# Optimization experiments

Measured on AMD Instinct MI355X. Metric: run time of the kernel, lower is better.

## Reference

```python
import jax, jax.numpy as jnp
import numpy as np
from jax import lax

C, K, EMB = 10, 32, 32
B, H, W = 32, 128, 128
DIRS = ((-1, 0), (1, 0), (0, -1), (0, 1))  # up, down, left, right


def _shift(x, dh, dw):
    # shift (B,H,W,...) by (dh,dw) with zero fill; x[b,h,w] <- x[b,h+dh,w+dw]
    pad = [(0, 0), (max(dh, 0), max(-dh, 0)), (max(dw, 0), max(-dw, 0))] + [(0, 0)] * (x.ndim - 3)
    xp = jnp.pad(x, pad)
    h0, w0 = max(-dh, 0), max(-dw, 0)
    return lax.dynamic_slice_in_dim(lax.dynamic_slice_in_dim(xp, h0, x.shape[1], 1), w0, x.shape[2], 2)


def conv(x, w, b):
    y = lax.conv_general_dilated(x, w, (1, 1), 'SAME',
                                 dimension_numbers=('NHWC', 'HWIO', 'NHWC'))
    return y + b


def small_cnn(x, w1, b1, w2, b2, w3, b3):
    x = jax.nn.relu(conv(x, w1, b1))
    x = jax.nn.relu(conv(x, w2, b2))
    return conv(x, w3, b3)


def neighbor_affinity(phi, tau=0.5):
    # phi: (B,H,W,D) -> w: (B,H,W,4) Gaussian feature affinity to 4 neighbors
    ones = jnp.ones(phi.shape[:3] + (1,), phi.dtype)
    ws = []
    for dh, dw in DIRS:
        nb = _shift(phi, dh, dw)
        valid = _shift(ones, dh, dw)[..., 0]
        d2 = jnp.sum((phi - nb) ** 2, axis=-1)
        ws.append(jnp.exp(-d2 / tau) * valid)
    return jnp.stack(ws, axis=-1)


def init_seeds_soft(Bv, Hv, Wv, Kv, dtype=jnp.float32):
    # K seeds on a gh x gw grid; soft assignment by squared distance
    gh = 4
    gw = Kv // gh
    sh = (jnp.arange(gh, dtype=dtype) + 0.5) * (Hv / gh)
    sw = (jnp.arange(gw, dtype=dtype) + 0.5) * (Wv / gw)
    seed_h = jnp.repeat(sh, gw)  # (K,)
    seed_w = jnp.tile(sw, gh)    # (K,)
    hh = jnp.arange(Hv, dtype=dtype)[:, None, None]
    ww = jnp.arange(Wv, dtype=dtype)[None, :, None]
    d2 = (hh - seed_h) ** 2 + (ww - seed_w) ** 2  # (H,W,K)
    sigma2 = (Hv / gh) * (Wv / gw)
    A = jax.nn.softmax(-d2 / sigma2, axis=-1)
    return jnp.broadcast_to(A[None], (Bv, Hv, Wv, Kv))


def soft_message_pass(A, w, beta=2.0):
    # aggregate neighbor assignments weighted by affinity, renormalize over K
    agg = jnp.zeros_like(A)
    for d, (dh, dw) in enumerate(DIRS):
        agg = agg + w[..., d:d + 1] * _shift(A, dh, dw)
    return jax.nn.softmax(beta * agg, axis=-1)


def soft_pool_features(G, A):
    # G:(B,H,W,C), A:(B,H,W,K) -> T:(B,K,1+2+C+4)
    Bv, Hv, Wv, Cv = G.shape
    eps = 1e-6
    mass = jnp.sum(A, axis=(1, 2)) + eps                      # (B,K)
    hh = (jnp.arange(Hv, dtype=G.dtype) + 0.5) / Hv
    ww = (jnp.arange(Wv, dtype=G.dtype) + 0.5) / Wv
    h_c = jnp.einsum('bhwk,h->bk', A, hh) / mass
    w_c = jnp.einsum('bhwk,w->bk', A, ww) / mass
    col = jnp.einsum('bhwk,bhwc->bkc', A, G) / mass[..., None]
    h2 = jnp.einsum('bhwk,h->bk', A, hh ** 2) / mass
    w2 = jnp.einsum('bhwk,w->bk', A, ww ** 2) / mass
    h_sd = jnp.sqrt(jax.nn.relu(h2 - h_c ** 2) + eps)
    w_sd = jnp.sqrt(jax.nn.relu(w2 - w_c ** 2) + eps)
    size = (mass / (Hv * Wv))[..., None]                      # (B,K,1)
    cen = jnp.stack([h_c, w_c], axis=-1)                      # (B,K,2)
    bbox = jnp.stack([h_c - h_sd, h_c + h_sd, w_c - w_sd, w_c + w_sd], axis=-1)
    return jnp.concatenate([size, cen, col, bbox], axis=-1)


def setup_inputs() -> dict:
    key = jax.random.key(0)
    ks = jax.random.split(key, 4)
    X = jax.random.randint(ks[0], (B, H, W), 0, C)
    w1 = jax.random.normal(ks[1], (3, 3, C, 32), jnp.float32) * (1.0 / np.sqrt(9 * C))
    w2 = jax.random.normal(ks[2], (3, 3, 32, 32), jnp.float32) * (1.0 / np.sqrt(9 * 32))
    w3 = jax.random.normal(ks[3], (1, 1, 32, EMB), jnp.float32) * (1.0 / np.sqrt(32))
    return {'X': X, 'w1': w1, 'b1': jnp.zeros((32,), jnp.float32),
            'w2': w2, 'b2': jnp.zeros((32,), jnp.float32),
            'w3': w3, 'b3': jnp.zeros((EMB,), jnp.float32)}


def reference(X, w1, b1, w2, b2, w3, b3):
    G = jax.nn.one_hot(X, C, dtype=jnp.float32)              # (B,H,W,C)
    phi = small_cnn(G, w1, b1, w2, b2, w3, b3)               # (B,H,W,EMB)
    w = neighbor_affinity(phi)                               # (B,H,W,4)
    A = init_seeds_soft(G.shape[0], G.shape[1], G.shape[2], K, G.dtype)
    for _ in range(8):
        A = soft_message_pass(A, w, beta=2.0)
    T = soft_pool_features(G, A)
    return A, T
```

## Files before the change

### kernel.cpp

```cpp
#include <hip/hip_runtime.h>
#include <math.h>

#define HD 128
#define WD 128
#define BB 32
#define KK 32
#define NPIX (BB*HD*WD)
#define PLANE ((size_t)NPIX*8)

typedef _Float16 f16;
typedef __attribute__((ext_vector_type(8))) _Float16 f16x8;
typedef __attribute__((ext_vector_type(4))) _Float16 f16x4;
typedef __attribute__((ext_vector_type(4))) float f32x4;

__device__ __forceinline__ int swz(int row, int g){
  return row*64 + (((g + (row >> 1)) & 3) << 4);
}

__device__ __forceinline__ float xexp2(float x){
#if __has_builtin(__builtin_amdgcn_exp2f)
  return __builtin_amdgcn_exp2f(x);
#else
  return exp2f(x);
#endif
}
__device__ __forceinline__ float xrcp(float x){
#if __has_builtin(__builtin_amdgcn_rcpf)
  return __builtin_amdgcn_rcpf(x);
#else
  return 1.f/x;
#endif
}
__device__ __forceinline__ f16x8 bc8(f16 x){
  f16x8 v;
  #pragma unroll
  for (int j = 0; j < 8; j++) v[j] = x;
  return v;
}

#define WSCALE 2.8853900817779268f

__global__ __launch_bounds__(512, 4) void cnnaff_kernel(
    const int* __restrict__ X,
    const float* __restrict__ w1, const float* __restrict__ b1,
    const float* __restrict__ w2, const float* __restrict__ b2,
    const float* __restrict__ w3, const float* __restrict__ b3,
    float* __restrict__ wb)
{
  __shared__ f16 sW1f[9*11*40];
  __shared__ int   sX[22*38];
  __shared__ float sB2[32], sB3[32];
  __shared__ f16 x1[720*32];
  __shared__ f16 w2t[9*32*32];
  __shared__ f16 w3t[32*32];

  const int tid = threadIdx.x;
  const int img = blockIdx.z;
  const int bh0 = blockIdx.y * 16;
  const int bw0 = blockIdx.x * 32;

  for (int i = tid; i < 9*11*32; i += 512) {
    int tap = i / 352, c = (i % 352) >> 5, oc = i & 31;
    float v = (c < 10) ? w1[tap*320 + c*32 + oc] : 0.f;
    if (tap == 4 && c < 10) v += b1[oc];
    sW1f[(tap*11 + c)*40 + oc] = (f16)v;
  }
  for (int i = tid; i < 9*32*32; i += 512) {
    int tap = i >> 10, ic = (i >> 5) & 31, oc = i & 31;
    int off = swz(tap*32 + oc, ic >> 3) + (ic & 7)*2;
    *(f16*)((char*)w2t + off) = (f16)w2[i];
  }
  for (int i = tid; i < 32*32; i += 512) {
    int ic = i >> 5, oe = i & 31;
    int off = swz(oe, ic >> 3) + (ic & 7)*2;
    *(f16*)((char*)w3t + off) = (f16)w3[i];
  }
  if (tid < 32) { sB2[tid] = b2[tid]; sB3[tid] = b3[tid]; }
  for (int i = tid; i < 22*38; i += 512) {
    int ti = i / 38, tj = i % 38;
    int gh = bh0 - 3 + ti, gw = bw0 - 3 + tj;
    sX[i] = (gh >= 0 && gh < HD && gw >= 0 && gw < WD) ? X[(img*HD + gh)*WD + gw] : 10;
  }
  __syncthreads();

  for (int p = tid; p < 720; p += 512) {
    int r = p / 36, c = p - r*36;
    int gh = bh0 - 2 + r, gw = bw0 - 2 + c;
    if (gh >= 0 && gh < HD && gw >= 0 && gw < WD) {
      f16x8 acc[4];
      {
        int cc = sX[r*38 + c];
        const f16* wr = &sW1f[cc*40];
        #pragma unroll
        for (int g = 0; g < 4; g++) acc[g] = *(const f16x8*)(wr + g*8);
      }
      #pragma unroll
      for (int tap = 1; tap < 9; tap++) {
        const int ti = tap/3, tj = tap%3;
        int cc = sX[(r+ti)*38 + c + tj];
        const f16* wr = &sW1f[(tap*11 + cc)*40];
        #pragma unroll
        for (int g = 0; g < 4; g++) acc[g] += *(const f16x8*)(wr + g*8);
      }
      #pragma unroll
      for (int g = 0; g < 4; g++) {
        f16x8 rr = acc[g];
        #pragma unroll
        for (int j = 0; j < 8; j++) rr[j] = (rr[j] > (f16)0.f) ? rr[j] : (f16)0.f;
        *(f16x8*)((char*)x1 + swz(p, g)) = rr;
      }
    } else {
      f16x8 z;
      #pragma unroll
      for (int j = 0; j < 8; j++) z[j] = (f16)0.f;
      #pragma unroll
      for (int g = 0; g < 4; g++) *(f16x8*)((char*)x1 + swz(p, g)) = z;
    }
  }
  __syncthreads();

  const int lane = tid & 63;
  const int wv   = tid >> 6;
  const int lr   = lane & 15;
  const int kg   = lane >> 4;
  const int mts  = wv * 5;

  int arow0[5];
  #pragma unroll
  for (int q = 0; q < 5; q++) {
    int px = (mts + q)*16 + lr;
    int pr = px / 34, pc = px - pr*34;
    arow0[q] = pr*36 + pc;
  }
  float b2v0 = sB2[lr], b2v1 = sB2[lr + 16];
  f32x4 acc[5][2];
  #pragma unroll
  for (int q = 0; q < 5; q++) {
    acc[q][0] = (f32x4){b2v0, b2v0, b2v0, b2v0};
    acc[q][1] = (f32x4){b2v1, b2v1, b2v1, b2v1};
  }
  #pragma unroll
  for (int tap = 0; tap < 9; tap++) {
    const int ti = tap/3, tj = tap%3;
    f16x8 bf0 = *(const f16x8*)((const char*)w2t + swz(tap*32 + lr,      kg));
    f16x8 bf1 = *(const f16x8*)((const char*)w2t + swz(tap*32 + lr + 16, kg));
    #pragma unroll
    for (int q = 0; q < 5; q++) {
      int row = arow0[q] + ti*36 + tj;
      f16x8 af = *(const f16x8*)((const char*)x1 + swz(row, kg));
      acc[q][0] = __builtin_amdgcn_mfma_f32_16x16x32_f16(af, bf0, acc[q][0], 0, 0, 0);
      acc[q][1] = __builtin_amdgcn_mfma_f32_16x16x32_f16(af, bf1, acc[q][1], 0, 0, 0);
    }
  }
  __syncthreads();

  #pragma unroll
  for (int q = 0; q < 5; q++)
    #pragma unroll
    for (int nt = 0; nt < 2; nt++) {
      int oc = nt*16 + lr;
      #pragma unroll
      for (int rg = 0; rg < 4; rg++) {
        int px = (mts + q)*16 + kg*4 + rg;
        int off = swz(px, oc >> 3) + (oc & 7)*2;
        *(f16*)((char*)x1 + off) = (f16)fmaxf(acc[q][nt][rg], 0.f);
      }
    }
  __syncthreads();

  {
    f16x8 cf0 = *(const f16x8*)((const char*)w3t + swz(lr,      kg));
    f16x8 cf1 = *(const f16x8*)((const char*)w3t + swz(lr + 16, kg));
    float b3v0 = sB3[lr], b3v1 = sB3[lr + 16];
    #pragma unroll
    for (int q = 0; q < 5; q++) {
      f16x8 af = *(const f16x8*)((const char*)x1 + swz((mts + q)*16 + lr, kg));
      f32x4 o0 = (f32x4){b3v0, b3v0, b3v0, b3v0};
      f32x4 o1 = (f32x4){b3v1, b3v1, b3v1, b3v1};
      o0 = __builtin_amdgcn_mfma_f32_16x16x32_f16(af, cf0, o0, 0, 0, 0);
      o1 = __builtin_amdgcn_mfma_f32_16x16x32_f16(af, cf1, o1, 0, 0, 0);
      #pragma unroll
      for (int rg = 0; rg < 4; rg++) {
        int px = (mts + q)*16 + kg*4 + rg;
        int offA = swz(px, lr >> 3) + (lr & 7)*2;
        int offB = swz(px, (lr+16) >> 3) + (lr & 7)*2;
        *(f16*)((char*)x1 + offA) = (f16)o0[rg];
        *(f16*)((char*)x1 + offB) = (f16)o1[rg];
      }
    }
  }
  __syncthreads();

  {
    int r2 = tid >> 5, c2 = tid & 31;
    int gh = bh0 + r2, gw = bw0 + c2;
    int qc = (r2+1)*34 + (c2+1);
    f16x8 c0 = *(const f16x8*)((const char*)x1 + swz(qc, 0));
    f16x8 c1 = *(const f16x8*)((const char*)x1 + swz(qc, 1));
    f16x8 c2v = *(const f16x8*)((const char*)x1 + swz(qc, 2));
    f16x8 c3 = *(const f16x8*)((const char*)x1 + swz(qc, 3));
    float4 out;
    #pragma unroll
    for (int d = 0; d < 4; d++) {
      int slot = (d == 0) ? qc + 34 : (d == 1) ? qc - 34 : (d == 2) ? qc + 1 : qc - 1;
      bool valid = (d == 0) ? (gh < HD-1) : (d == 1) ? (gh > 0) : (d == 2) ? (gw < WD-1) : (gw > 0);
      f16x8 n0 = *(const f16x8*)((const char*)x1 + swz(slot, 0));
      f16x8 n1 = *(const f16x8*)((const char*)x1 + swz(slot, 1));
      f16x8 n2 = *(const f16x8*)((const char*)x1 + swz(slot, 2));
      f16x8 n3 = *(const f16x8*)((const char*)x1 + swz(slot, 3));
      f16x8 d0 = c0 - n0; f16x8 s = d0*d0;
      f16x8 d1 = c1 - n1; s += d1*d1;
      f16x8 d2 = c2v - n2; s += d2*d2;
      f16x8 d3 = c3 - n3; s += d3*d3;
      float d2f = 0.f;
      #pragma unroll
      for (int j = 0; j < 8; j++) d2f += (float)s[j];
      float v = valid ? WSCALE * xexp2(-WSCALE * d2f) : 0.f;
      if (d == 0) out.x = v; else if (d == 1) out.y = v; else if (d == 2) out.z = v; else out.w = v;
    }
    ((float4*)wb)[(size_t)img*HD*WD + gh*WD + gw] = out;
  }
}

__device__ __forceinline__ void a0_accum2(float* a, int hh, int ww, float wt) {
  const float C = 0.0028177637517362567f;
  float eh[4], ew[8];
  float sh = 0.f, sw = 0.f;
  const float fh = (float)hh, fw = (float)ww;
  #pragma unroll
  for (int kh = 0; kh < 4; kh++) { float d = fh - (float)(kh*32+16); eh[kh] = xexp2(-d*d*C); sh += eh[kh]; }
  #pragma unroll
  for (int kw = 0; kw < 8; kw++) { float d = fw - (float)(kw*16+8); ew[kw] = xexp2(-d*d*C); sw += ew[kw]; }
  float sc = wt * xrcp(sh * sw);
  #pragma unroll
  for (int kh = 0; kh < 4; kh++) {
    float ehs = eh[kh] * sc;
    #pragma unroll
    for (int kw = 0; kw < 8; kw++) a[kh*8+kw] = fmaf(ehs, ew[kw], a[kh*8+kw]);
  }
}

template<int FIRST, int LAST>
__global__ __launch_bounds__(512, 6) void mp2_kernel(const f16* __restrict__ Ain,
                                                     const float* __restrict__ wb,
                                                     f16* __restrict__ Aout,
                                                     float* __restrict__ AoutF) {
  __shared__ f16 amid[612*32];

  const int blk  = blockIdx.x;
  const int xcd  = blk & 7;
  const int q    = blk >> 3;
  const int img  = xcd + ((q >> 5) << 3);
  const int tile = q & 31;
  const int th0  = (tile >> 2) * 16;
  const int tw0  = (tile & 3) * 32;
  const size_t ibase = (size_t)img * HD * WD;

  for (int p = threadIdx.x; p < 612; p += 512) {
    int r = p / 34, cc = p - r*34;
    int gh = th0 - 1 + r, gw = tw0 - 1 + cc;
    bool inimg = ((unsigned)gh < (unsigned)HD) && ((unsigned)gw < (unsigned)WD);
    int ghc = min(max(gh, 0), HD-1), gwc = min(max(gw, 0), WD-1);
    float4 wd = inimg ? ((const float4*)wb)[ibase + gh*WD + gw] : make_float4(0.f,0.f,0.f,0.f);
    int hu = ghc + ((ghc < HD-1) ? 1 : 0);
    int hd = ghc - ((ghc > 0)    ? 1 : 0);
    int wl = gwc + ((gwc < WD-1) ? 1 : 0);
    int wr = gwc - ((gwc > 0)    ? 1 : 0);

    float s = 0.f;
    f16x8 pe[4];
    if (FIRST) {
      float a[32];
      #pragma unroll
      for (int k = 0; k < 32; k++) a[k] = 0.f;
      a0_accum2(a, hu, gwc, wd.x);
      a0_accum2(a, hd, gwc, wd.y);
      a0_accum2(a, ghc, wl, wd.z);
      a0_accum2(a, ghc, wr, wd.w);
      #pragma unroll
      for (int g = 0; g < 4; g++)
        #pragma unroll
        for (int j = 0; j < 8; j++) { float e = xexp2(a[g*8+j]); s += e; pe[g][j] = (f16)e; }
    } else {
      const size_t iu_ = ibase + (size_t)hu*WD + gwc;
      const size_t id_ = ibase + (size_t)hd*WD + gwc;
      const size_t il_ = ibase + (size_t)ghc*WD + wl;
      const size_t ir_ = ibase + (size_t)ghc*WD + wr;
      f16x8 w0 = bc8((f16)wd.x), w1 = bc8((f16)wd.y), w2 = bc8((f16)wd.z), w3 = bc8((f16)wd.w);
      #pragma unroll
      for (int g = 0; g < 4; g++) {
        const f16* pg = Ain + (size_t)g*PLANE;
        f16x8 v0 = *(const f16x8*)(pg + iu_*8);
        f16x8 v1 = *(const f16x8*)(pg + id_*8);
        f16x8 v2 = *(const f16x8*)(pg + il_*8);
        f16x8 v3 = *(const f16x8*)(pg + ir_*8);
        f16x8 agg = v0*w0 + v1*w1 + v2*w2 + v3*w3;
        #pragma unroll
        for (int j = 0; j < 8; j++) { float e = xexp2((float)agg[j]); s += e; pe[g][j] = (f16)e; }
      }
    }
    f16x8 iv = bc8((f16)xrcp(s));
    #pragma unroll
    for (int g = 0; g < 4; g++)
      *(f16x8*)((char*)amid + swz(p, g)) = pe[g]*iv;
  }
  __syncthreads();

  {
    int r2 = threadIdx.x >> 5, c2 = threadIdx.x & 31;
    int gh = th0 + r2, gw = tw0 + c2;
    int rm = r2 + 1, cm = c2 + 1;
    float4 wd = ((const float4*)wb)[ibase + gh*WD + gw];
    int q0 = (rm + ((gh < HD-1) ? 1 : 0))*34 + cm;
    int q1 = (rm - ((gh > 0)    ? 1 : 0))*34 + cm;
    int q2 = rm*34 + cm + ((gw < WD-1) ? 1 : 0);
    int q3 = rm*34 + cm - ((gw > 0)    ? 1 : 0);
    f16x8 w0 = bc8((f16)wd.x), w1 = bc8((f16)wd.y), w2 = bc8((f16)wd.z), w3 = bc8((f16)wd.w);
    float s = 0.f;
    f16x8 pe[4];
    #pragma unroll
    for (int g = 0; g < 4; g++) {
      f16x8 v0 = *(const f16x8*)((const char*)amid + swz(q0, g));
      f16x8 v1 = *(const f16x8*)((const char*)amid + swz(q1, g));
      f16x8 v2 = *(const f16x8*)((const char*)amid + swz(q2, g));
      f16x8 v3 = *(const f16x8*)((const char*)amid + swz(q3, g));
      f16x8 agg = v0*w0 + v1*w1 + v2*w2 + v3*w3;
      #pragma unroll
      for (int j = 0; j < 8; j++) { float e = xexp2((float)agg[j]); s += e; pe[g][j] = (f16)e; }
    }
    f16x8 iv = bc8((f16)xrcp(s));
    #pragma unroll
    for (int g = 0; g < 4; g++) pe[g] = pe[g]*iv;

    if (!LAST) {
      size_t opix = ibase + (size_t)gh*WD + gw;
      #pragma unroll
      for (int g = 0; g < 4; g++)
        *(f16x8*)(Aout + (size_t)g*PLANE + opix*8) = pe[g];
    } else {
      __syncthreads();
      f16* planes = amid;
      #pragma unroll
      for (int g = 0; g < 4; g++)
        *(f16x8*)((char*)planes + (g*513 + threadIdx.x)*16) = pe[g];
      __syncthreads();
      float* obase = AoutF + ((size_t)(img*HD + th0)*WD + tw0)*32;
      #pragma unroll
      for (int rep = 0; rep < 8; rep++) {
        int flat = rep*512 + threadIdx.x;
        int row = flat >> 8;
        int within = flat & 255;
        int pxr = within >> 3;
        int kq = within & 7;
        int g = kq >> 1, half = kq & 1;
        int pxl = row*32 + pxr;
        f16x4 v = *(const f16x4*)((const char*)planes + (g*513 + pxl)*16 + half*8);
        float4 o;
        o.x = (float)v[0]; o.y = (float)v[1]; o.z = (float)v[2]; o.w = (float)v[3];
        *(float4*)(obase + (size_t)row*WD*32 + pxr*32 + kq*4) = o;
      }
    }
  }
}

__global__ __launch_bounds__(256) void pool1_kernel(const float* __restrict__ A,
                                                    const int* __restrict__ X,
                                                    float* __restrict__ part) {
  const int b = blockIdx.x, cy = blockIdx.y;
  const int k = threadIdx.x & 31, sub = threadIdx.x >> 5;
  const int h = cy*4 + (sub >> 1);
  const int w0 = (sub & 1) * 64;
  const float hh = ((float)h + 0.5f) * (1.f/128.f);
  float s0 = 0.f, sw = 0.f, sw2 = 0.f;
  float col[10];
  #pragma unroll
  for (int c = 0; c < 10; c++) col[c] = 0.f;
  const float* Arow = A + ((size_t)((b*HD + h)*WD + w0))*32 + k;
  const int*   Xrow = X + (b*HD + h)*WD + w0;
  for (int w = 0; w < 64; w++) {
    float a  = Arow[(size_t)w*32];
    float ww = ((float)(w + w0) + 0.5f) * (1.f/128.f);
    s0 += a; sw = fmaf(ww, a, sw); sw2 = fmaf(ww*ww, a, sw2);
    int x = Xrow[w];
    #pragma unroll
    for (int c = 0; c < 10; c++) col[c] += (x == c) ? a : 0.f;
  }
  __shared__ float red[8][32][15];
  float vals[15];
  vals[0] = s0; vals[1] = hh*s0; vals[2] = sw; vals[3] = hh*hh*s0; vals[4] = sw2;
  #pragma unroll
  for (int c = 0; c < 10; c++) vals[5+c] = col[c];
  #pragma unroll
  for (int q = 0; q < 15; q++) red[sub][k][q] = vals[q];
  __syncthreads();
  if (sub == 0) {
    #pragma unroll
    for (int q = 0; q < 15; q++) {
      float v = 0.f;
      #pragma unroll
      for (int s2 = 0; s2 < 8; s2++) v += red[s2][k][q];
      part[(((size_t)b*32 + cy)*32 + k)*15 + q] = v;
    }
  }
}

__global__ __launch_bounds__(256) void pool2_kernel(const float* __restrict__ part,
                                                    float* __restrict__ T) {
  const int t = blockIdx.x * 256 + threadIdx.x;
  if (t >= BB*KK) return;
  const int b = t >> 5, k = t & 31;
  float s[15];
  #pragma unroll
  for (int q = 0; q < 15; q++) s[q] = 0.f;
  for (int cy = 0; cy < 32; cy++) {
    const float* p = part + (((size_t)b*32 + cy)*32 + k)*15;
    #pragma unroll
    for (int q = 0; q < 15; q++) s[q] += p[q];
  }
  float mass = s[0] + 1e-6f;
  float inv  = 1.f / mass;
  float h_c = s[1]*inv, w_c = s[2]*inv, h2 = s[3]*inv, w2 = s[4]*inv;
  float h_sd = sqrtf(fmaxf(h2 - h_c*h_c, 0.f) + 1e-6f);
  float w_sd = sqrtf(fmaxf(w2 - w_c*w_c, 0.f) + 1e-6f);
  float* o = T + (size_t)t*17;
  o[0] = mass * (1.f/16384.f);
  o[1] = h_c; o[2] = w_c;
  #pragma unroll
  for (int c = 0; c < 10; c++) o[3+c] = s[5+c]*inv;
  o[13] = h_c - h_sd; o[14] = h_c + h_sd; o[15] = w_c - w_sd; o[16] = w_c + w_sd;
}

extern "C" void kernel_launch(void* const* d_in, const int* in_sizes, int n_in,
                              void* d_out, int out_size, void* d_ws, size_t ws_size,
                              hipStream_t stream) {
  const int*   X  = (const int*)d_in[0];
  const float* w1 = (const float*)d_in[1];
  const float* b1 = (const float*)d_in[2];
  const float* w2 = (const float*)d_in[3];
  const float* b2 = (const float*)d_in[4];
  const float* w3 = (const float*)d_in[5];
  const float* b3 = (const float*)d_in[6];

  float* out   = (float*)d_out;
  float* A_out = out;
  float* T_out = out + (size_t)NPIX * KK;

  char*  ws   = (char*)d_ws;
  f16*   bufA = (f16*)ws;
  f16*   bufB = (f16*)(ws + (size_t)32*1024*1024);
  float* wb   = (float*)(ws + (size_t)64*1024*1024);
  float* part = (float*)ws;

  cnnaff_kernel<<<dim3(WD/32, HD/16, BB), 512, 0, stream>>>(X, w1, b1, w2, b2, w3, b3, wb);

  mp2_kernel<1,0><<<1024, 512, 0, stream>>>(nullptr, wb, bufA, nullptr);
  mp2_kernel<0,0><<<1024, 512, 0, stream>>>(bufA, wb, bufB, nullptr);
  mp2_kernel<0,0><<<1024, 512, 0, stream>>>(bufB, wb, bufA, nullptr);
  mp2_kernel<0,1><<<1024, 512, 0, stream>>>(bufA, wb, nullptr, A_out);

  pool1_kernel<<<dim3(BB, 32), 256, 0, stream>>>(A_out, X, part);
  pool2_kernel<<<(BB*KK + 255)/256, 256, 0, stream>>>(part, T_out);
}
```

Before: 236.2 us.

## Fuse four message-pass iterations per kernel using halo-recompute in shared memory

```diff
diff --git a/kernel.cpp b/kernel.cpp
--- a/kernel.cpp
+++ b/kernel.cpp
@@ -222,30 +222,79 @@
   }
 }
 
-__device__ __forceinline__ void a0_accum2(float* a, int hh, int ww, float wt) {
+__device__ __forceinline__ void a0_row(float fh, float* eh, float& s){
   const float C = 0.0028177637517362567f;
-  float eh[4], ew[8];
-  float sh = 0.f, sw = 0.f;
-  const float fh = (float)hh, fw = (float)ww;
-  #pragma unroll
-  for (int kh = 0; kh < 4; kh++) { float d = fh - (float)(kh*32+16); eh[kh] = xexp2(-d*d*C); sh += eh[kh]; }
-  #pragma unroll
-  for (int kw = 0; kw < 8; kw++) { float d = fw - (float)(kw*16+8); ew[kw] = xexp2(-d*d*C); sw += ew[kw]; }
-  float sc = wt * xrcp(sh * sw);
-  #pragma unroll
-  for (int kh = 0; kh < 4; kh++) {
-    float ehs = eh[kh] * sc;
-    #pragma unroll
-    for (int kw = 0; kw < 8; kw++) a[kh*8+kw] = fmaf(ehs, ew[kw], a[kh*8+kw]);
-  }
+  s = 0.f;
+  #pragma unroll
+  for (int kh = 0; kh < 4; kh++){ float d = fh - (float)(kh*32+16); eh[kh] = xexp2(-d*d*C); s += eh[kh]; }
+}
+__device__ __forceinline__ void a0_col(float fw, float* ew, float& s){
+  const float C = 0.0028177637517362567f;
+  s = 0.f;
+  #pragma unroll
+  for (int kw = 0; kw < 8; kw++){ float d = fw - (float)(kw*16+8); ew[kw] = xexp2(-d*d*C); s += ew[kw]; }
+}
+
+__device__ __forceinline__ void mp_px_reg(const f16* __restrict__ amid, int slot,
+                                          int du, int dd, int dl, int dr,
+                                          float4 wd, f16x8* out) {
+  f16x8 w0 = bc8((f16)wd.x), w1 = bc8((f16)wd.y), w2 = bc8((f16)wd.z), w3 = bc8((f16)wd.w);
+  float s = 0.f;
+  f16x8 pe[4];
+  #pragma unroll
+  for (int g = 0; g < 4; g++) {
+    f16x8 v0 = *(const f16x8*)((const char*)amid + swz(slot + du, g));
+    f16x8 v1 = *(const f16x8*)((const char*)amid + swz(slot + dd, g));
+    f16x8 v2 = *(const f16x8*)((const char*)amid + swz(slot + dl, g));
+    f16x8 v3 = *(const f16x8*)((const char*)amid + swz(slot + dr, g));
+    f16x8 agg = v0*w0 + v1*w1 + v2*w2 + v3*w3;
+    #pragma unroll
+    for (int j = 0; j < 8; j++) { float e = xexp2((float)agg[j]); s += e; pe[g][j] = (f16)e; }
+  }
+  f16x8 iv = bc8((f16)xrcp(s));
+  #pragma unroll
+  for (int g = 0; g < 4; g++) out[g] = pe[g]*iv;
+}
+
+__device__ __forceinline__ void mp_px_a0(int gh, int gw, float4 wd, f16x8* out) {
+  int ghc = min(max(gh, 0), HD-1), gwc = min(max(gw, 0), WD-1);
+  int hu = ghc + ((ghc < HD-1) ? 1 : 0);
+  int hd = ghc - ((ghc > 0)    ? 1 : 0);
+  int wl = gwc + ((gwc < WD-1) ? 1 : 0);
+  int wr = gwc - ((gwc > 0)    ? 1 : 0);
+  float eh[4], ehu[4], ehd[4], ew[8], ewl[8], ewr[8];
+  float Sh, Shu, Shd, Sw, Swl, Swr;
+  a0_row((float)ghc, eh, Sh); a0_row((float)hu, ehu, Shu); a0_row((float)hd, ehd, Shd);
+  a0_col((float)gwc, ew, Sw); a0_col((float)wl, ewl, Swl); a0_col((float)wr, ewr, Swr);
+  float cu = wd.x * xrcp(Shu * Sw);
+  float cd = wd.y * xrcp(Shd * Sw);
+  float cl = wd.z * xrcp(Sh * Swl);
+  float cr = wd.w * xrcp(Sh * Swr);
+  float c1[4], c2[8];
+  #pragma unroll
+  for (int kh = 0; kh < 4; kh++) c1[kh] = cu*ehu[kh] + cd*ehd[kh];
+  #pragma unroll
+  for (int kw = 0; kw < 8; kw++) c2[kw] = cl*ewl[kw] + cr*ewr[kw];
+  float s = 0.f;
+  f16x8 pe[4];
+  #pragma unroll
+  for (int g = 0; g < 4; g++)
+    #pragma unroll
+    for (int j = 0; j < 8; j++) {
+      float aa = fmaf(c1[g], ew[j], eh[g]*c2[j]);
+      float e = xexp2(aa); s += e; pe[g][j] = (f16)e;
+    }
+  f16x8 iv = bc8((f16)xrcp(s));
+  #pragma unroll
+  for (int g = 0; g < 4; g++) out[g] = pe[g]*iv;
 }
 
 template<int FIRST, int LAST>
-__global__ __launch_bounds__(512, 6) void mp2_kernel(const f16* __restrict__ Ain,
+__global__ __launch_bounds__(512, 4) void mp4_kernel(const f16* __restrict__ Ain,
                                                      const float* __restrict__ wb,
                                                      f16* __restrict__ Aout,
                                                      float* __restrict__ AoutF) {
-  __shared__ f16 amid[612*32];
+  __shared__ f16 amid[960*32];
 
   const int blk  = blockIdx.x;
   const int xcd  = blk & 7;
@@ -256,81 +305,114 @@
   const int tw0  = (tile & 3) * 32;
   const size_t ibase = (size_t)img * HD * WD;
 
-  for (int p = threadIdx.x; p < 612; p += 512) {
-    int r = p / 34, cc = p - r*34;
-    int gh = th0 - 1 + r, gw = tw0 - 1 + cc;
-    bool inimg = ((unsigned)gh < (unsigned)HD) && ((unsigned)gw < (unsigned)WD);
-    int ghc = min(max(gh, 0), HD-1), gwc = min(max(gw, 0), WD-1);
-    float4 wd = inimg ? ((const float4*)wb)[ibase + gh*WD + gw] : make_float4(0.f,0.f,0.f,0.f);
-    int hu = ghc + ((ghc < HD-1) ? 1 : 0);
-    int hd = ghc - ((ghc > 0)    ? 1 : 0);
-    int wl = gwc + ((gwc < WD-1) ? 1 : 0);
-    int wr = gwc - ((gwc > 0)    ? 1 : 0);
-
-    float s = 0.f;
+  if (!FIRST) {
+    for (int t = threadIdx.x; t < 3840; t += 512) {
+      int g = t / 960, slot = t - g*960;
+      int sr = slot / 40, sc = slot - sr*40;
+      int gh = min(max(th0 + sr - 4, 0), HD-1);
+      int gw = min(max(tw0 + sc - 4, 0), WD-1);
+      f16x8 v = *(const f16x8*)(Ain + (size_t)g*PLANE + (ibase + (size_t)gh*WD + gw)*8);
+      *(f16x8*)((char*)amid + swz(slot, g)) = v;
+    }
+    __syncthreads();
+  }
+
+  {
+    constexpr int N = 22*38;
+    f16x8 r0[4], r1[4];
+    int slot0, slot1 = 0;
+    const bool own1 = (threadIdx.x + 512) < N;
+    {
+      int p = threadIdx.x;
+      int r = p / 38, c = p - r*38;
+      int gh = th0 - 3 + r, gw = tw0 - 3 + c;
+      slot0 = (r + 1)*40 + (c + 1);
+      bool inimg = ((unsigned)gh < (unsigned)HD) && ((unsigned)gw < (unsigned)WD);
+      float4 wd = inimg ? ((const float4*)wb)[ibase + gh*WD + gw] : make_float4(0.f,0.f,0.f,0.f);
+      if (FIRST) mp_px_a0(gh, gw, wd, r0);
+      else {
+        int du = (gh < HD-1) ? 40 : 0, dd = (gh > 0) ? -40 : 0;
+        int dl = (gw < WD-1) ? 1 : 0,  dr = (gw > 0) ? -1 : 0;
+        mp_px_reg(amid, slot0, du, dd, dl, dr, wd, r0);
+      }
+    }
+    if (own1) {
+      int p = threadIdx.x + 512;
+      int r = p / 38, c = p - r*38;
+      int gh = th0 - 3 + r, gw = tw0 - 3 + c;
+      slot1 = (r + 1)*40 + (c + 1);
+      bool inimg = ((unsigned)gh < (unsigned)HD) && ((unsigned)gw < (unsigned)WD);
+      float4 wd = inimg ? ((const float4*)wb)[ibase + gh*WD + gw] : make_float4(0.f,0.f,0.f,0.f);
+      if (FIRST) mp_px_a0(gh, gw, wd, r1);
+      else {
+        int du = (gh < HD-1) ? 40 : 0, dd = (gh > 0) ? -40 : 0;
+        int dl = (gw < WD-1) ? 1 : 0,  dr = (gw > 0) ? -1 : 0;
+        mp_px_reg(amid, slot1, du, dd, dl, dr, wd, r1);
+      }
+    }
+    __syncthreads();
+    #pragma unroll
+    for (int g = 0; g < 4; g++) *(f16x8*)((char*)amid + swz(slot0, g)) = r0[g];
+    if (own1) {
+      #pragma unroll
+      for (int g = 0; g < 4; g++) *(f16x8*)((char*)amid + swz(slot1, g)) = r1[g];
+    }
+    __syncthreads();
+  }
+
+  #define MP_ITER(HH, WW, OO)                                                        \
+  {                                                                                  \
+    constexpr int N = (HH)*(WW);                                                     \
+    f16x8 r0[4], r1[4];                                                              \
+    int slot0, slot1 = 0;                                                            \
+    const bool own1 = (threadIdx.x + 512) < N;                                       \
+    {                                                                                \
+      int p = threadIdx.x;                                                           \
+      int r = p / (WW), c = p - r*(WW);                                              \
+      int gh = th0 + (OO) + r, gw = tw0 + (OO) + c;                                  \
+      slot0 = (r + (OO) + 4)*40 + (c + (OO) + 4);                                    \
+      bool inimg = ((unsigned)gh < (unsigned)HD) && ((unsigned)gw < (unsigned)WD);   \
+      float4 wd = inimg ? ((const float4*)wb)[ibase + gh*WD + gw]                    \
+                        : make_float4(0.f,0.f,0.f,0.f);                              \
+      int du = (gh < HD-1) ? 40 : 0, dd = (gh > 0) ? -40 : 0;                        \
+      int dl = (gw < WD-1) ? 1 : 0,  dr = (gw > 0) ? -1 : 0;                         \
+      mp_px_reg(amid, slot0, du, dd, dl, dr, wd, r0);                                \
+    }                                                                                \
+    if (own1) {                                                                      \
+      int p = threadIdx.x + 512;                                                     \
+      int r = p / (WW), c = p - r*(WW);                                              \
+      int gh = th0 + (OO) + r, gw = tw0 + (OO) + c;                                  \
+      slot1 = (r + (OO) + 4)*40 + (c + (OO) + 4);                                    \
+      bool inimg = ((unsigned)gh < (unsigned)HD) && ((unsigned)gw < (unsigned)WD);   \
+      float4 wd = inimg ? ((const float4*)wb)[ibase + gh*WD + gw]                    \
+                        : make_float4(0.f,0.f,0.f,0.f);                              \
+      int du = (gh < HD-1) ? 40 : 0, dd = (gh > 0) ? -40 : 0;                        \
+      int dl = (gw < WD-1) ? 1 : 0,  dr = (gw > 0) ? -1 : 0;                         \
+      mp_px_reg(amid, slot1, du, dd, dl, dr, wd, r1);                                \
+    }                                                                                \
+    __syncthreads();                                                                 \
+    _Pragma("unroll")                                                                \
+    for (int g = 0; g < 4; g++) *(f16x8*)((char*)amid + swz(slot0, g)) = r0[g];      \
+    if (own1) {                                                                      \
+      _Pragma("unroll")                                                              \
+      for (int g = 0; g < 4; g++) *(f16x8*)((char*)amid + swz(slot1, g)) = r1[g];    \
+    }                                                                                \
+    __syncthreads();                                                                 \
+  }
+
+  MP_ITER(20, 36, -2)
+  MP_ITER(18, 34, -1)
+  #undef MP_ITER
+
+  {
+    int r = threadIdx.x >> 5, c = threadIdx.x & 31;
+    int gh = th0 + r, gw = tw0 + c;
+    int slot = (r + 4)*40 + (c + 4);
+    float4 wd = ((const float4*)wb)[ibase + gh*WD + gw];
+    int du = (gh < HD-1) ? 40 : 0, dd = (gh > 0) ? -40 : 0;
+    int dl = (gw < WD-1) ? 1 : 0,  dr = (gw > 0) ? -1 : 0;
     f16x8 pe[4];
-    if (FIRST) {
-      float a[32];
-      #pragma unroll
-      for (int k = 0; k < 32; k++) a[k] = 0.f;
-      a0_accum2(a, hu, gwc, wd.x);
-      a0_accum2(a, hd, gwc, wd.y);
-      a0_accum2(a, ghc, wl, wd.z);
-      a0_accum2(a, ghc, wr, wd.w);
-      #pragma unroll
-      for (int g = 0; g < 4; g++)
-        #pragma unroll
-        for (int j = 0; j < 8; j++) { float e = xexp2(a[g*8+j]); s += e; pe[g][j] = (f16)e; }
-    } else {
-      const size_t iu_ = ibase + (size_t)hu*WD + gwc;
-      const size_t id_ = ibase + (size_t)hd*WD + gwc;
-      const size_t il_ = ibase + (size_t)ghc*WD + wl;
-      const size_t ir_ = ibase + (size_t)ghc*WD + wr;
-      f16x8 w0 = bc8((f16)wd.x), w1 = bc8((f16)wd.y), w2 = bc8((f16)wd.z), w3 = bc8((f16)wd.w);
-      #pragma unroll
-      for (int g = 0; g < 4; g++) {
-        const f16* pg = Ain + (size_t)g*PLANE;
-        f16x8 v0 = *(const f16x8*)(pg + iu_*8);
-        f16x8 v1 = *(const f16x8*)(pg + id_*8);
-        f16x8 v2 = *(const f16x8*)(pg + il_*8);
-        f16x8 v3 = *(const f16x8*)(pg + ir_*8);
-        f16x8 agg = v0*w0 + v1*w1 + v2*w2 + v3*w3;
-        #pragma unroll
-        for (int j = 0; j < 8; j++) { float e = xexp2((float)agg[j]); s += e; pe[g][j] = (f16)e; }
-      }
-    }
-    f16x8 iv = bc8((f16)xrcp(s));
-    #pragma unroll
-    for (int g = 0; g < 4; g++)
-      *(f16x8*)((char*)amid + swz(p, g)) = pe[g]*iv;
-  }
-  __syncthreads();
-
-  {
-    int r2 = threadIdx.x >> 5, c2 = threadIdx.x & 31;
-    int gh = th0 + r2, gw = tw0 + c2;
-    int rm = r2 + 1, cm = c2 + 1;
-    float4 wd = ((const float4*)wb)[ibase + gh*WD + gw];
-    int q0 = (rm + ((gh < HD-1) ? 1 : 0))*34 + cm;
-    int q1 = (rm - ((gh > 0)    ? 1 : 0))*34 + cm;
-    int q2 = rm*34 + cm + ((gw < WD-1) ? 1 : 0);
-    int q3 = rm*34 + cm - ((gw > 0)    ? 1 : 0);
-    f16x8 w0 = bc8((f16)wd.x), w1 = bc8((f16)wd.y), w2 = bc8((f16)wd.z), w3 = bc8((f16)wd.w);
-    float s = 0.f;
-    f16x8 pe[4];
-    #pragma unroll
-    for (int g = 0; g < 4; g++) {
-      f16x8 v0 = *(const f16x8*)((const char*)amid + swz(q0, g));
-      f16x8 v1 = *(const f16x8*)((const char*)amid + swz(q1, g));
-      f16x8 v2 = *(const f16x8*)((const char*)amid + swz(q2, g));
-      f16x8 v3 = *(const f16x8*)((const char*)amid + swz(q3, g));
-      f16x8 agg = v0*w0 + v1*w1 + v2*w2 + v3*w3;
-      #pragma unroll
-      for (int j = 0; j < 8; j++) { float e = xexp2((float)agg[j]); s += e; pe[g][j] = (f16)e; }
-    }
-    f16x8 iv = bc8((f16)xrcp(s));
-    #pragma unroll
-    for (int g = 0; g < 4; g++) pe[g] = pe[g]*iv;
+    mp_px_reg(amid, slot, du, dd, dl, dr, wd, pe);
 
     if (!LAST) {
       size_t opix = ibase + (size_t)gh*WD + gw;
@@ -447,16 +529,13 @@
 
   char*  ws   = (char*)d_ws;
   f16*   bufA = (f16*)ws;
-  f16*   bufB = (f16*)(ws + (size_t)32*1024*1024);
-  float* wb   = (float*)(ws + (size_t)64*1024*1024);
+  float* wb   = (float*)(ws + (size_t)32*1024*1024);
   float* part = (float*)ws;
 
   cnnaff_kernel<<<dim3(WD/32, HD/16, BB), 512, 0, stream>>>(X, w1, b1, w2, b2, w3, b3, wb);
 
-  mp2_kernel<1,0><<<1024, 512, 0, stream>>>(nullptr, wb, bufA, nullptr);
-  mp2_kernel<0,0><<<1024, 512, 0, stream>>>(bufA, wb, bufB, nullptr);
-  mp2_kernel<0,0><<<1024, 512, 0, stream>>>(bufB, wb, bufA, nullptr);
-  mp2_kernel<0,1><<<1024, 512, 0, stream>>>(bufA, wb, nullptr, A_out);
+  mp4_kernel<1,0><<<1024, 512, 0, stream>>>(nullptr, wb, bufA, nullptr);
+  mp4_kernel<0,1><<<1024, 512, 0, stream>>>(bufA, wb, nullptr, A_out);
 
   pool1_kernel<<<dim3(BB, 32), 256, 0, stream>>>(A_out, X, part);
   pool2_kernel<<<(BB*KK + 255)/256, 256, 0, stream>>>(part, T_out);
```

Measured after the change: 251.6 us. 1.07x slower.
